# Kernel tuning notes

Measured on AMD Instinct MI355X. Metric: run time of the kernel, lower is better.

Reference implementation:

```python
import jax, jax.numpy as jnp
import numpy as np

B, T, D_MODEL, WINDOW = 2, 2048, 512, 32


def setup_inputs() -> dict:
    key = jax.random.key(0)
    ks = jax.random.split(key, 5)
    s = 1.0 / np.sqrt(D_MODEL)
    x = jax.random.normal(ks[0], (B, T, D_MODEL), jnp.float32)
    # torch.nn.Linear convention: weight [out_features, in_features], y = x @ W.T + b
    w_qkv = jax.random.uniform(ks[1], (3 * D_MODEL, D_MODEL), jnp.float32, -s, s)
    b_qkv = jax.random.uniform(ks[2], (3 * D_MODEL,), jnp.float32, -s, s)
    w_proj = jax.random.uniform(ks[3], (D_MODEL, D_MODEL), jnp.float32, -s, s)
    b_proj = jax.random.uniform(ks[4], (D_MODEL,), jnp.float32, -s, s)
    return {"x": x, "w_qkv": w_qkv, "b_qkv": b_qkv, "w_proj": w_proj, "b_proj": b_proj}


def reference(x, w_qkv, b_qkv, w_proj, b_proj):
    Bb, Tt, C = x.shape
    qkv = x @ w_qkv.T + b_qkv                      # [B,T,3C]
    q, k, v = jnp.split(qkv, 3, axis=-1)           # each [B,T,C]
    W = 2 * WINDOW - 1                             # non-causal window span [t-w+1, t+w-1]
    offs = jnp.arange(W) - (WINDOW - 1)            # [W]
    idx = jnp.arange(Tt)[:, None] + offs[None, :]  # [T,W] absolute key positions
    valid = (idx >= 0) & (idx < Tt)                # mask out-of-range window slots
    idx_c = jnp.clip(idx, 0, Tt - 1)
    k_win = k[:, idx_c]                            # [B,T,W,C]
    v_win = v[:, idx_c]                            # [B,T,W,C]
    scale = jnp.asarray(C, x.dtype) ** 0.5
    scores = jnp.einsum('btc,btwc->btw', q, k_win) / scale
    scores = jnp.where(valid[None], scores, -jnp.inf)
    p = jax.nn.softmax(scores, axis=-1)            # [B,T,W]
    out = jnp.einsum('btw,btwc->btc', p, v_win)    # [B,T,C]
    return out @ w_proj.T + b_proj
```

## Files before the change

kernel.cpp:

```cpp
#include <hip/hip_runtime.h>
#include <math.h>

#define BB 2
#define TT 2048
#define CC 512
#define WIN 32
#define WSZ 63
#define MM (BB * TT)

typedef __attribute__((ext_vector_type(8))) short short8;
typedef __attribute__((ext_vector_type(4))) float floatx4;

__device__ inline unsigned short bf16_rn(float f) {
  unsigned u = __builtin_bit_cast(unsigned, f);
  u += 0x7fff + ((u >> 16) & 1);
  return (unsigned short)(u >> 16);
}
__device__ inline unsigned pack_bf16x2(float lo, float hi) {
  return (unsigned)bf16_rn(lo) | ((unsigned)bf16_rn(hi) << 16);
}

#define NX  (MM * CC)
#define NWQ (3 * CC * CC)
#define NWP (CC * CC)

__global__ __launch_bounds__(256) void convert_bf16(
    const float* __restrict__ x, const float* __restrict__ wq,
    const float* __restrict__ wp, ushort* __restrict__ xb,
    ushort* __restrict__ wqb, ushort* __restrict__ wpb) {
  const size_t e = ((size_t)blockIdx.x * 256 + threadIdx.x) * 8;
  const float* src;
  ushort* dst;
  size_t off;
  if (e < NX) { src = x; dst = xb; off = e; }
  else if (e < NX + NWQ) { src = wq; dst = wqb; off = e - NX; }
  else { src = wp; dst = wpb; off = e - NX - NWQ; }
  float4 v0 = ((const float4*)(src + off))[0];
  float4 v1 = ((const float4*)(src + off))[1];
  uint4 o;
  o.x = pack_bf16x2(v0.x, v0.y);
  o.y = pack_bf16x2(v0.z, v0.w);
  o.z = pack_bf16x2(v1.x, v1.y);
  o.w = pack_bf16x2(v1.z, v1.w);
  *(uint4*)(dst + off) = o;
}

#define PSTR 264
#define VSTR 136

template <int BM, typename OT>
__global__ __launch_bounds__(256) void gemm_panel(
    const ushort* __restrict__ A, const ushort* __restrict__ B,
    const float* __restrict__ bias, OT* __restrict__ C,
    ushort* __restrict__ VT, int M, int N) {
  constexpr int MIW = BM / 64;
  __shared__ __align__(16) ushort Bs[64 * PSTR];

  const int tid = threadIdx.x;
  const int lane = tid & 63;
  const int wave = tid >> 6;
  const int m0 = blockIdx.y * BM;
  const int n0 = blockIdx.x * 64;
  const int wm = wave * (BM / 4);
  const int mlane = lane & 15, quad = lane >> 4;

  floatx4 acc[MIW][4];
#pragma unroll
  for (int i = 0; i < MIW; ++i)
#pragma unroll
    for (int j = 0; j < 4; ++j) acc[i][j] = (floatx4){0.f, 0.f, 0.f, 0.f};

  for (int h = 0; h < 2; ++h) {
    if (h) __syncthreads();
#pragma unroll
    for (int i = 0; i < 8; ++i) {
      const int idx = tid + 256 * i;
      const int r = idx >> 5, kc = (idx & 31) * 8;
      *(uint4*)(&Bs[r * PSTR + kc]) =
          *(const uint4*)(B + (size_t)(n0 + r) * CC + h * 256 + kc);
    }
    __syncthreads();
#pragma unroll
    for (int ks = 0; ks < 8; ++ks) {
      short8 bfr[4];
#pragma unroll
      for (int ni = 0; ni < 4; ++ni)
        bfr[ni] = *(const short8*)(&Bs[(ni * 16 + mlane) * PSTR + ks * 32 + quad * 8]);
#pragma unroll
      for (int mi = 0; mi < MIW; ++mi) {
        short8 af = *(const short8*)(
            A + (size_t)(m0 + wm + mi * 16 + mlane) * CC + h * 256 + ks * 32 + quad * 8);
#pragma unroll
        for (int ni = 0; ni < 4; ++ni)
          acc[mi][ni] = __builtin_amdgcn_mfma_f32_16x16x32_bf16(af, bfr[ni], acc[mi][ni], 0, 0, 0);
      }
    }
  }

  const bool vpath = (VT != nullptr) && (n0 >= 1024);
  if (!vpath) {
#pragma unroll
    for (int ni = 0; ni < 4; ++ni) {
      const int n = n0 + ni * 16 + mlane;
      const float bn = bias[n];
#pragma unroll
      for (int mi = 0; mi < MIW; ++mi) {
        const int mbase = m0 + wm + mi * 16 + quad * 4;
#pragma unroll
        for (int r = 0; r < 4; ++r) {
          float val = acc[mi][ni][r] + bn;
          if constexpr (sizeof(OT) == 2)
            ((ushort*)C)[(size_t)(mbase + r) * N + n] = bf16_rn(val);
          else
            ((float*)C)[(size_t)(mbase + r) * N + n] = val;
        }
      }
    }
  } else if constexpr (BM == 128) {
    ushort* Vt = Bs;
    __syncthreads();
#pragma unroll
    for (int ni = 0; ni < 4; ++ni) {
      const int n_l = ni * 16 + mlane;
      const float bn = bias[n0 + n_l];
#pragma unroll
      for (int mi = 0; mi < MIW; ++mi) {
        const int m_l = wm + mi * 16 + quad * 4;
        ushort4 pk;
        pk.x = bf16_rn(acc[mi][ni][0] + bn);
        pk.y = bf16_rn(acc[mi][ni][1] + bn);
        pk.z = bf16_rn(acc[mi][ni][2] + bn);
        pk.w = bf16_rn(acc[mi][ni][3] + bn);
        *(ushort4*)(&Vt[n_l * VSTR + m_l]) = pk;
      }
    }
    __syncthreads();
#pragma unroll
    for (int i = 0; i < 4; ++i) {
      const int idx = tid + 256 * i;
      const int n_l = idx >> 4, mo = (idx & 15) * 8;
      *(uint4*)(VT + (size_t)(n0 - 1024 + n_l) * M + m0 + mo) =
          *(const uint4*)(&Vt[n_l * VSTR + mo]);
    }
  }
}

#define ATILE 16
#define SLD 84
#define PLD 104

__global__ __launch_bounds__(256) void attn_mfma(
    const ushort* __restrict__ qkv, const ushort* __restrict__ vT,
    ushort* __restrict__ out) {
  __shared__ __align__(16) float s_s[16 * SLD];
  __shared__ __align__(16) ushort p_s[16 * PLD];

  const int tid = threadIdx.x;
  const int wave = tid >> 6, lane = tid & 63;
  const int mlane = lane & 15, quad = lane >> 4;
  const int tile = ((blockIdx.x & 7) << 5) | (blockIdx.x >> 3);
  const int bt0 = tile * ATILE;
  const int b = bt0 / TT, t0 = bt0 % TT;
  const ushort* qbase = qkv + (size_t)b * TT * (3 * CC);

  const ushort* qrow  = qbase + (ptrdiff_t)(t0 + mlane) * (3 * CC);
  const ushort* krow0 = qbase + (ptrdiff_t)(t0 - 32 + wave * 16 + mlane) * (3 * CC) + CC;
  const ushort* krow1 = qbase + (ptrdiff_t)(t0 - 32 + 64 + mlane) * (3 * CC) + CC;
  floatx4 sacc0 = (floatx4){0.f, 0.f, 0.f, 0.f};
  floatx4 sacc1 = (floatx4){0.f, 0.f, 0.f, 0.f};
#pragma unroll
  for (int ks = 0; ks < 16; ++ks) {
    short8 a  = *(const short8*)(qrow + ks * 32 + quad * 8);
    short8 b0 = *(const short8*)(krow0 + ks * 32 + quad * 8);
    sacc0 = __builtin_amdgcn_mfma_f32_16x16x32_bf16(a, b0, sacc0, 0, 0, 0);
    if (wave == 0) {
      short8 b1 = *(const short8*)(krow1 + ks * 32 + quad * 8);
      sacc1 = __builtin_amdgcn_mfma_f32_16x16x32_bf16(a, b1, sacc1, 0, 0, 0);
    }
  }

#pragma unroll
  for (int r = 0; r < 4; ++r)
    s_s[(quad * 4 + r) * SLD + wave * 16 + mlane] = sacc0[r];
  if (wave == 0) {
#pragma unroll
    for (int r = 0; r < 4; ++r)
      s_s[(quad * 4 + r) * SLD + 64 + mlane] = sacc1[r];
  }
  __syncthreads();

  {
    const int row = tid >> 4, li = tid & 15;
    const float inv_scale = 0.044194173824159216f;
    float e[5];
    float mx = -INFINITY;
#pragma unroll
    for (int i = 0; i < 5; ++i) {
      const int r = li + 16 * i;
      const int j = r - 1 - row;
      const int src = t0 - 32 + r;
      const bool valid = (j >= 0) && (j < WSZ) && (src >= 0) && (src < TT);
      e[i] = valid ? s_s[row * SLD + r] * inv_scale : -INFINITY;
      mx = fmaxf(mx, e[i]);
    }
    mx = fmaxf(mx, __shfl_xor(mx, 1)); mx = fmaxf(mx, __shfl_xor(mx, 2));
    mx = fmaxf(mx, __shfl_xor(mx, 4)); mx = fmaxf(mx, __shfl_xor(mx, 8));
    float sum = 0.f;
#pragma unroll
    for (int i = 0; i < 5; ++i) {
      e[i] = (e[i] == -INFINITY) ? 0.f : __expf(e[i] - mx);
      sum += e[i];
    }
    sum += __shfl_xor(sum, 1); sum += __shfl_xor(sum, 2);
    sum += __shfl_xor(sum, 4); sum += __shfl_xor(sum, 8);
    const float rs = 1.f / sum;
#pragma unroll
    for (int i = 0; i < 5; ++i)
      p_s[row * PLD + li + 16 * i] = bf16_rn(e[i] * rs);
    if (li < 8) {
      p_s[row * PLD + 80 + li] = 0;
      p_s[row * PLD + 88 + li] = 0;
      p_s[row * PLD + 96 + li] = 0;
    }
  }
  __syncthreads();

  short8 pa[3];
#pragma unroll
  for (int ks = 0; ks < 3; ++ks)
    pa[ks] = *(const short8*)(&p_s[mlane * PLD + ks * 32 + quad * 8]);

  const ptrdiff_t mcol0 = (ptrdiff_t)b * TT + t0 - 32;
#pragma unroll 2
  for (int nt8 = 0; nt8 < 8; ++nt8) {
    const int nt = wave * 8 + nt8;
    const ushort* vrow = vT + (ptrdiff_t)(nt * 16 + mlane) * MM + mcol0;
    floatx4 o = (floatx4){0.f, 0.f, 0.f, 0.f};
#pragma unroll
    for (int ks = 0; ks < 3; ++ks) {
      short8 bv = *(const short8*)(vrow + ks * 32 + quad * 8);
      o = __builtin_amdgcn_mfma_f32_16x16x32_bf16(pa[ks], bv, o, 0, 0, 0);
    }
#pragma unroll
    for (int r = 0; r < 4; ++r)
      out[(size_t)(bt0 + quad * 4 + r) * CC + nt * 16 + mlane] = bf16_rn(o[r]);
  }
}

extern "C" void kernel_launch(void* const* d_in, const int* in_sizes, int n_in,
                              void* d_out, int out_size, void* d_ws, size_t ws_size,
                              hipStream_t stream) {
  const float* x      = (const float*)d_in[0];
  const float* w_qkv  = (const float*)d_in[1];
  const float* b_qkv  = (const float*)d_in[2];
  const float* w_proj = (const float*)d_in[3];
  const float* b_proj = (const float*)d_in[4];
  float* outp = (float*)d_out;

  ushort* base  = (ushort*)d_ws;
  ushort* qkv   = base + 131072;
  ushort* attn  = qkv + (size_t)MM * 3 * CC;
  ushort* xb    = attn + (size_t)MM * CC;
  ushort* wqb   = xb + (size_t)NX;
  ushort* wpb   = wqb + (size_t)NWQ;
  ushort* vTg   = wpb + (size_t)NWP;
  ushort* vT    = vTg + 64;

  convert_bf16<<<(NX + NWQ + NWP) / (256 * 8), 256, 0, stream>>>(x, w_qkv, w_proj, xb, wqb, wpb);
  {
    dim3 grid((3 * CC) / 64, MM / 128);
    gemm_panel<128, ushort><<<grid, 256, 0, stream>>>(xb, wqb, b_qkv, qkv, vT, MM, 3 * CC);
  }
  attn_mfma<<<MM / ATILE, 256, 0, stream>>>(qkv, vT, attn);
  {
    dim3 grid(CC / 64, MM / 64);
    gemm_panel<64, float><<<grid, 256, 0, stream>>>(attn, wpb, b_proj, outp, nullptr, MM, CC);
  }
}
```

Measured before the change: 107.4 us.

## Store all bf16 operands in MFMA fragment-tiled layouts for coalesced loads

Converts x and both weight matrices into blocked layouts during the bf16 conversion. The layouts group 8-element k chunks by row tile, so each MFMA fragment load becomes one contiguous 16-byte access per lane. The QKV GEMM now writes Q, K and V directly in those tiled layouts, which removes the LDS-staged transpose of V. The attention output is also written tiled for the projection GEMM. This replaces strided row-major global and LDS accesses with linear ones, at the cost of scattered 2-byte stores in the epilogues and more complex indexing.

```diff
diff --git a/kernel.cpp b/kernel.cpp
--- a/kernel.cpp
+++ b/kernel.cpp
@@ -32,11 +32,21 @@
   const float* src;
   ushort* dst;
   size_t off;
-  if (e < NX) { src = x; dst = xb; off = e; }
-  else if (e < NX + NWQ) { src = wq; dst = wqb; off = e - NX; }
-  else { src = wp; dst = wpb; off = e - NX - NWQ; }
-  float4 v0 = ((const float4*)(src + off))[0];
-  float4 v1 = ((const float4*)(src + off))[1];
+  if (e < NX) {
+    const size_t m = e >> 9, k = e & 511;
+    src = x + e; dst = xb;
+    off = (m >> 4) * 8192 + (k >> 3) * 128 + (m & 15) * 8;
+  } else if (e < NX + NWQ) {
+    const size_t i = e - NX, n = i >> 9, k = i & 511;
+    src = wq + i; dst = wqb;
+    off = (n >> 6) * 32768 + (k >> 3) * 512 + (n & 63) * 8;
+  } else {
+    const size_t i = e - NX - NWQ, n = i >> 9, k = i & 511;
+    src = wp + i; dst = wpb;
+    off = (n >> 6) * 32768 + (k >> 3) * 512 + (n & 63) * 8;
+  }
+  float4 v0 = ((const float4*)src)[0];
+  float4 v1 = ((const float4*)src)[1];
   uint4 o;
   o.x = pack_bf16x2(v0.x, v0.y);
   o.y = pack_bf16x2(v0.z, v0.w);
@@ -45,16 +55,13 @@
   *(uint4*)(dst + off) = o;
 }
 
-#define PSTR 264
-#define VSTR 136
-
 template <int BM, typename OT>
 __global__ __launch_bounds__(256) void gemm_panel(
-    const ushort* __restrict__ A, const ushort* __restrict__ B,
+    const ushort* __restrict__ A, const ushort* __restrict__ Bt,
     const float* __restrict__ bias, OT* __restrict__ C,
-    ushort* __restrict__ VT, int M, int N) {
+    ushort* __restrict__ VT, int N) {
   constexpr int MIW = BM / 64;
-  __shared__ __align__(16) ushort Bs[64 * PSTR];
+  __shared__ __align__(16) ushort Bs[16384];
 
   const int tid = threadIdx.x;
   const int lane = tid & 63;
@@ -70,14 +77,13 @@
 #pragma unroll
     for (int j = 0; j < 4; ++j) acc[i][j] = (floatx4){0.f, 0.f, 0.f, 0.f};
 
+  const ushort* bpanel = Bt + (size_t)(n0 >> 6) * 32768;
   for (int h = 0; h < 2; ++h) {
     if (h) __syncthreads();
 #pragma unroll
     for (int i = 0; i < 8; ++i) {
       const int idx = tid + 256 * i;
-      const int r = idx >> 5, kc = (idx & 31) * 8;
-      *(uint4*)(&Bs[r * PSTR + kc]) =
-          *(const uint4*)(B + (size_t)(n0 + r) * CC + h * 256 + kc);
+      *(uint4*)(&Bs[idx * 8]) = *(const uint4*)(bpanel + h * 16384 + idx * 8);
     }
     __syncthreads();
 #pragma unroll
@@ -85,11 +91,12 @@
       short8 bfr[4];
 #pragma unroll
       for (int ni = 0; ni < 4; ++ni)
-        bfr[ni] = *(const short8*)(&Bs[(ni * 16 + mlane) * PSTR + ks * 32 + quad * 8]);
+        bfr[ni] = *(const short8*)(&Bs[((ks * 4 + quad) * 64 + ni * 16 + mlane) * 8]);
 #pragma unroll
       for (int mi = 0; mi < MIW; ++mi) {
-        short8 af = *(const short8*)(
-            A + (size_t)(m0 + wm + mi * 16 + mlane) * CC + h * 256 + ks * 32 + quad * 8);
+        const size_t aoff = (size_t)((m0 + wm) / 16 + mi) * 8192 +
+                            (size_t)(h * 32 + ks * 4 + quad) * 128 + mlane * 8;
+        short8 af = *(const short8*)(A + aoff);
 #pragma unroll
         for (int ni = 0; ni < 4; ++ni)
           acc[mi][ni] = __builtin_amdgcn_mfma_f32_16x16x32_bf16(af, bfr[ni], acc[mi][ni], 0, 0, 0);
@@ -97,8 +104,43 @@
     }
   }
 
-  const bool vpath = (VT != nullptr) && (n0 >= 1024);
-  if (!vpath) {
+  if constexpr (sizeof(OT) == 2) {
+    if (n0 < 1024) {
+      ushort* dst = (ushort*)C + (n0 < 512 ? 0 : 2097152);
+      const int c0 = n0 & 511;
+#pragma unroll
+      for (int ni = 0; ni < 4; ++ni) {
+        const int c = c0 + ni * 16 + mlane;
+        const float bn = bias[n0 + ni * 16 + mlane];
+        const int kpo = (c >> 3) * 128 + (c & 7);
+#pragma unroll
+        for (int mi = 0; mi < MIW; ++mi) {
+          const size_t mb =
+              (size_t)((m0 + wm) / 16 + mi) * 8192 + kpo + (size_t)quad * 32;
+#pragma unroll
+          for (int r = 0; r < 4; ++r)
+            dst[mb + r * 8] = bf16_rn(acc[mi][ni][r] + bn);
+        }
+      }
+    } else {
+#pragma unroll
+      for (int ni = 0; ni < 4; ++ni) {
+        const int nv = (n0 - 1024) + ni * 16 + mlane;
+        const float bn = bias[n0 + ni * 16 + mlane];
+#pragma unroll
+        for (int mi = 0; mi < MIW; ++mi) {
+          const int mb = m0 + wm + mi * 16 + quad * 4;
+          ushort4 pk;
+          pk.x = bf16_rn(acc[mi][ni][0] + bn);
+          pk.y = bf16_rn(acc[mi][ni][1] + bn);
+          pk.z = bf16_rn(acc[mi][ni][2] + bn);
+          pk.w = bf16_rn(acc[mi][ni][3] + bn);
+          *(ushort4*)(&VT[(size_t)(nv >> 4) * 65536 + (size_t)(mb >> 3) * 128 +
+                          (nv & 15) * 8 + (mb & 7)]) = pk;
+        }
+      }
+    }
+  } else {
 #pragma unroll
     for (int ni = 0; ni < 4; ++ni) {
       const int n = n0 + ni * 16 + mlane;
@@ -107,51 +149,19 @@
       for (int mi = 0; mi < MIW; ++mi) {
         const int mbase = m0 + wm + mi * 16 + quad * 4;
 #pragma unroll
-        for (int r = 0; r < 4; ++r) {
-          float val = acc[mi][ni][r] + bn;
-          if constexpr (sizeof(OT) == 2)
-            ((ushort*)C)[(size_t)(mbase + r) * N + n] = bf16_rn(val);
-          else
-            ((float*)C)[(size_t)(mbase + r) * N + n] = val;
-        }
-      }
-    }
-  } else if constexpr (BM == 128) {
-    ushort* Vt = Bs;
-    __syncthreads();
-#pragma unroll
-    for (int ni = 0; ni < 4; ++ni) {
-      const int n_l = ni * 16 + mlane;
-      const float bn = bias[n0 + n_l];
-#pragma unroll
-      for (int mi = 0; mi < MIW; ++mi) {
-        const int m_l = wm + mi * 16 + quad * 4;
-        ushort4 pk;
-        pk.x = bf16_rn(acc[mi][ni][0] + bn);
-        pk.y = bf16_rn(acc[mi][ni][1] + bn);
-        pk.z = bf16_rn(acc[mi][ni][2] + bn);
-        pk.w = bf16_rn(acc[mi][ni][3] + bn);
-        *(ushort4*)(&Vt[n_l * VSTR + m_l]) = pk;
-      }
-    }
-    __syncthreads();
-#pragma unroll
-    for (int i = 0; i < 4; ++i) {
-      const int idx = tid + 256 * i;
-      const int n_l = idx >> 4, mo = (idx & 15) * 8;
-      *(uint4*)(VT + (size_t)(n0 - 1024 + n_l) * M + m0 + mo) =
-          *(const uint4*)(&Vt[n_l * VSTR + mo]);
-    }
-  }
-}
-
-#define ATILE 16
+        for (int r = 0; r < 4; ++r)
+          ((float*)C)[(size_t)(mbase + r) * N + n] = acc[mi][ni][r] + bn;
+      }
+    }
+  }
+}
+
 #define SLD 84
 #define PLD 104
 
 __global__ __launch_bounds__(256) void attn_mfma(
-    const ushort* __restrict__ qkv, const ushort* __restrict__ vT,
-    ushort* __restrict__ out) {
+    const ushort* __restrict__ Qb, const ushort* __restrict__ Kb,
+    const ushort* __restrict__ VT, ushort* __restrict__ outT) {
   __shared__ __align__(16) float s_s[16 * SLD];
   __shared__ __align__(16) ushort p_s[16 * PLD];
 
@@ -159,22 +169,21 @@
   const int wave = tid >> 6, lane = tid & 63;
   const int mlane = lane & 15, quad = lane >> 4;
   const int tile = ((blockIdx.x & 7) << 5) | (blockIdx.x >> 3);
-  const int bt0 = tile * ATILE;
-  const int b = bt0 / TT, t0 = bt0 % TT;
-  const ushort* qbase = qkv + (size_t)b * TT * (3 * CC);
-
-  const ushort* qrow  = qbase + (ptrdiff_t)(t0 + mlane) * (3 * CC);
-  const ushort* krow0 = qbase + (ptrdiff_t)(t0 - 32 + wave * 16 + mlane) * (3 * CC) + CC;
-  const ushort* krow1 = qbase + (ptrdiff_t)(t0 - 32 + 64 + mlane) * (3 * CC) + CC;
+  const int bt0 = tile * 16;
+  const int t0 = bt0 % TT;
+
+  const ushort* qp  = Qb + (size_t)tile * 8192 + quad * 128 + mlane * 8;
+  const ushort* kp0 = Kb + (ptrdiff_t)(tile - 2 + wave) * 8192 + quad * 128 + mlane * 8;
+  const ushort* kp1 = Kb + (ptrdiff_t)(tile + 2) * 8192 + quad * 128 + mlane * 8;
   floatx4 sacc0 = (floatx4){0.f, 0.f, 0.f, 0.f};
   floatx4 sacc1 = (floatx4){0.f, 0.f, 0.f, 0.f};
 #pragma unroll
   for (int ks = 0; ks < 16; ++ks) {
-    short8 a  = *(const short8*)(qrow + ks * 32 + quad * 8);
-    short8 b0 = *(const short8*)(krow0 + ks * 32 + quad * 8);
+    short8 a  = *(const short8*)(qp + ks * 512);
+    short8 b0 = *(const short8*)(kp0 + ks * 512);
     sacc0 = __builtin_amdgcn_mfma_f32_16x16x32_bf16(a, b0, sacc0, 0, 0, 0);
     if (wave == 0) {
-      short8 b1 = *(const short8*)(krow1 + ks * 32 + quad * 8);
+      short8 b1 = *(const short8*)(kp1 + ks * 512);
       sacc1 = __builtin_amdgcn_mfma_f32_16x16x32_bf16(a, b1, sacc1, 0, 0, 0);
     }
   }
@@ -230,20 +239,22 @@
   for (int ks = 0; ks < 3; ++ks)
     pa[ks] = *(const short8*)(&p_s[mlane * PLD + ks * 32 + quad * 8]);
 
-  const ptrdiff_t mcol0 = (ptrdiff_t)b * TT + t0 - 32;
+  const ptrdiff_t mp0 = ((ptrdiff_t)bt0 - 32) >> 3;
+  const size_t ob = (size_t)tile * 8192 + (size_t)(mlane >> 3) * 128 +
+                    (size_t)quad * 32 + (mlane & 7);
 #pragma unroll 2
   for (int nt8 = 0; nt8 < 8; ++nt8) {
     const int nt = wave * 8 + nt8;
-    const ushort* vrow = vT + (ptrdiff_t)(nt * 16 + mlane) * MM + mcol0;
+    const ushort* vb = VT + (ptrdiff_t)nt * 65536 + (mp0 + quad) * 128 + mlane * 8;
     floatx4 o = (floatx4){0.f, 0.f, 0.f, 0.f};
 #pragma unroll
     for (int ks = 0; ks < 3; ++ks) {
-      short8 bv = *(const short8*)(vrow + ks * 32 + quad * 8);
+      short8 bv = *(const short8*)(vb + ks * 512);
       o = __builtin_amdgcn_mfma_f32_16x16x32_bf16(pa[ks], bv, o, 0, 0, 0);
     }
 #pragma unroll
     for (int r = 0; r < 4; ++r)
-      out[(size_t)(bt0 + quad * 4 + r) * CC + nt * 16 + mlane] = bf16_rn(o[r]);
+      outT[ob + (size_t)nt * 256 + r * 8] = bf16_rn(o[r]);
   }
 }
 
@@ -258,22 +269,26 @@
   float* outp = (float*)d_out;
 
   ushort* base  = (ushort*)d_ws;
-  ushort* qkv   = base + 131072;
-  ushort* attn  = qkv + (size_t)MM * 3 * CC;
-  ushort* xb    = attn + (size_t)MM * CC;
-  ushort* wqb   = xb + (size_t)NX;
-  ushort* wpb   = wqb + (size_t)NWQ;
-  ushort* vTg   = wpb + (size_t)NWP;
-  ushort* vT    = vTg + 64;
-
-  convert_bf16<<<(NX + NWQ + NWP) / (256 * 8), 256, 0, stream>>>(x, w_qkv, w_proj, xb, wqb, wpb);
+  ushort* Qb    = base + 131072;
+  ushort* Kb    = Qb + 2097152;
+  ushort* attnT = Kb + 2097152;
+  ushort* xbT   = attnT + 2097152;
+  ushort* wqbT  = xbT + 2097152;
+  ushort* wpbT  = wqbT + 786432;
+  ushort* vTg   = wpbT + 262144;
+  ushort* vT    = vTg + 1024;
+
+  convert_bf16<<<(NX + NWQ + NWP) / (256 * 8), 256, 0, stream>>>(
+      x, w_qkv, w_proj, xbT, wqbT, wpbT);
   {
     dim3 grid((3 * CC) / 64, MM / 128);
-    gemm_panel<128, ushort><<<grid, 256, 0, stream>>>(xb, wqb, b_qkv, qkv, vT, MM, 3 * CC);
-  }
-  attn_mfma<<<MM / ATILE, 256, 0, stream>>>(qkv, vT, attn);
+    gemm_panel<128, ushort><<<grid, 256, 0, stream>>>(
+        xbT, wqbT, b_qkv, Qb, vT, 3 * CC);
+  }
+  attn_mfma<<<256, 256, 0, stream>>>(Qb, Kb, vT, attnT);
   {
     dim3 grid(CC / 64, MM / 64);
-    gemm_panel<64, float><<<grid, 256, 0, stream>>>(attn, wpb, b_proj, outp, nullptr, MM, CC);
-  }
-}
+    gemm_panel<64, float><<<grid, 256, 0, stream>>>(
+        attnT, wpbT, b_proj, outp, nullptr, CC);
+  }
+}
```

Result: slower. 112.2 us (+4.5%).
